# Kernel optimization log

Measured on AMD Instinct MI355X. Metric: run time of the kernel, lower is better.

## Reference

```python
import jax, jax.numpy as jnp
import numpy as np


def setup_inputs() -> dict:
    key = jax.random.key(0)
    k1, k2 = jax.random.split(key)
    B, H, W, C = 8, 192, 640, 64
    c1 = jax.random.normal(k1, (B, H, W, C), dtype=jnp.float32)
    warp = jax.random.normal(k2, (B, H, W, C), dtype=jnp.float32)
    return {"c1": c1, "warp": warp, "search_range": 2}


def reference(c1, warp, search_range):
    # c1, warp: [B, H, W, C]; pad warp along width by search_range on both sides
    padded = jnp.pad(warp, ((0, 0), (0, 0), (search_range, search_range), (0, 0)))
    width = c1.shape[2]
    max_offset = 2 * search_range + 1  # small fixed loop (5 offsets)
    cost_vol = [
        jnp.mean(c1 * padded[:, :, i:width + i, :], axis=3, keepdims=True)
        for i in range(max_offset)
    ]
    # cost_curve: [B, H, W, C + max_offset]
    return jnp.concatenate([c1] + cost_vol, axis=3)
```

## Files before the change

### kernel.cpp

```cpp
#include <hip/hip_runtime.h>


typedef float f32x4 __attribute__((ext_vector_type(4)));

#define WIDTH 640
#define CH 64
#define NOFF 5
#define OUTC 69
#define REC_F4 69
#define NPIX (8 * 192 * 640)
#define NPAIR (NPIX / 8)
#define NITER 8
#define BDIM 256
#define WPB (BDIM / 64)
#define NBLOCKS (NPAIR / (WPB * NITER))
#define PAIRS_PER_ROW (WIDTH / 8)

__device__ __forceinline__ float row_reduce_sum16_lane0(float v) {
    union { float f; int i; } a, b;
    a.f = v;
    b.i = __builtin_amdgcn_update_dpp(0, a.i, 0x101, 0xF, 0xF, true); a.f += b.f;
    b.i = __builtin_amdgcn_update_dpp(0, a.i, 0x102, 0xF, 0xF, true); a.f += b.f;
    b.i = __builtin_amdgcn_update_dpp(0, a.i, 0x104, 0xF, 0xF, true); a.f += b.f;
    b.i = __builtin_amdgcn_update_dpp(0, a.i, 0x108, 0xF, 0xF, true); a.f += b.f;
    return a.f;
}

struct Frag {
    f32x4 a0, a1;
    f32x4 b0[NOFF], b1[NOFF];
};

__global__ __launch_bounds__(BDIM) void StereoCostVolume_kernel(
    const float* __restrict__ c1,
    const float* __restrict__ warp,
    float* __restrict__ out)
{
    __shared__ f32x4 lds[WPB * 2 * REC_F4];

    const int t   = threadIdx.x;
    const int wid = t >> 6;
    const int l   = t & 63;
    const int px  = l >> 4;
    const int c4  = l & 15;

    const f32x4* c1f4   = (const f32x4*)c1;
    const f32x4* warpf4 = (const f32x4*)warp;
    f32x4*       outf4  = (f32x4*)out;

    const int wave  = blockIdx.x * WPB + wid;
    const int pbase = wave * NITER;
    const int rp0   = pbase % PAIRS_PER_ROW;
    const bool leftw  = (rp0 == 0);
    const bool rightw = (rp0 == PAIRS_PER_ROW - NITER);

    const int base0 = (pbase * 8 + px) * 16 + c4;

    float* rec0w = (float*)&lds[(wid * 2 + 0) * REC_F4];
    float* rec1w = (float*)&lds[(wid * 2 + 1) * REC_F4];
    const f32x4* rec0r = (const f32x4*)rec0w;
    const f32x4* rec1r = (const f32x4*)rec1w;

    auto LOAD = [&](int it, Frag& F) {
        const int base = base0 + it * 128;
        F.a0 = __builtin_nontemporal_load(&c1f4[base]);
        F.a1 = __builtin_nontemporal_load(&c1f4[base + 64]);
        const bool edge = (leftw && it == 0) || (rightw && it == NITER - 1);
        if (!edge) {
            #pragma unroll
            for (int d = 0; d < NOFF; ++d) {
                F.b0[d] = warpf4[base + (d - 2) * 16];
                F.b1[d] = warpf4[base + 64 + (d - 2) * 16];
            }
        } else {
            const int w0 = (rp0 + it) * 8 + px;
            #pragma unroll
            for (int d = 0; d < NOFF; ++d) {
                const int ww0 = w0 + d - 2;
                const int ww1 = ww0 + 4;
                F.b0[d] = (ww0 >= 0 && ww0 < WIDTH) ? warpf4[base + (d - 2) * 16]
                                                    : f32x4{0.f, 0.f, 0.f, 0.f};
                F.b1[d] = (ww1 >= 0 && ww1 < WIDTH) ? warpf4[base + 64 + (d - 2) * 16]
                                                    : f32x4{0.f, 0.f, 0.f, 0.f};
            }
        }
    };

    auto PROC = [&](int it, const Frag& F) {
        float s0[NOFF], s1[NOFF];
        #pragma unroll
        for (int d = 0; d < NOFF; ++d) {
            const float acc0 = F.a0.x * F.b0[d].x + F.a0.y * F.b0[d].y
                             + F.a0.z * F.b0[d].z + F.a0.w * F.b0[d].w;
            const float acc1 = F.a1.x * F.b1[d].x + F.a1.y * F.b1[d].y
                             + F.a1.z * F.b1[d].z + F.a1.w * F.b1[d].w;
            s0[d] = row_reduce_sum16_lane0(acc0);
            s1[d] = row_reduce_sum16_lane0(acc1);
        }
        const int fb = px * OUTC + c4 * 4;
        rec0w[fb + 0] = F.a0.x; rec0w[fb + 1] = F.a0.y;
        rec0w[fb + 2] = F.a0.z; rec0w[fb + 3] = F.a0.w;
        rec1w[fb + 0] = F.a1.x; rec1w[fb + 1] = F.a1.y;
        rec1w[fb + 2] = F.a1.z; rec1w[fb + 3] = F.a1.w;
        if (c4 == 0) {
            #pragma unroll
            for (int d = 0; d < NOFF; ++d) {
                rec0w[px * OUTC + CH + d] = s0[d] * 0.015625f;
                rec1w[px * OUTC + CH + d] = s1[d] * 0.015625f;
            }
        }
        __builtin_amdgcn_wave_barrier();

        const int ob = (pbase + it) * (2 * REC_F4);
        __builtin_nontemporal_store(rec0r[l], &outf4[ob + l]);
        __builtin_nontemporal_store(rec1r[l], &outf4[ob + REC_F4 + l]);
        if (l < REC_F4 - 64) {
            __builtin_nontemporal_store(rec0r[64 + l], &outf4[ob + 64 + l]);
            __builtin_nontemporal_store(rec1r[64 + l], &outf4[ob + REC_F4 + 64 + l]);
        }
        __builtin_amdgcn_wave_barrier();
    };

    Frag X, Y;
    LOAD(0, X);
    #pragma unroll
    for (int ii = 0; ii < NITER; ii += 2) {
        LOAD(ii + 1, Y);
        PROC(ii, X);
        if (ii + 2 < NITER) LOAD(ii + 2, X);
        PROC(ii + 1, Y);
    }
}

extern "C" void kernel_launch(void* const* d_in, const int* in_sizes, int n_in,
                              void* d_out, int out_size, void* d_ws, size_t ws_size,
                              hipStream_t stream) {
    const float* c1   = (const float*)d_in[0];
    const float* warp = (const float*)d_in[1];
    float* out = (float*)d_out;

    StereoCostVolume_kernel<<<NBLOCKS, BDIM, 0, stream>>>(c1, warp, out);
}
```

Baseline: 125.4 us.

## Issue loads via inline asm with manual vmcnt waits for explicit double-buffering

Replaces the compiler-generated global loads with inline-asm global_load_dwordx4 using immediate offsets. The per-iteration pipeline is now driven by explicit s_waitcnt vmcnt values and sched barriers, so the next fragment's loads stay in flight while the current one is processed. Edge loads are turned into clamped, always-valid addresses, and out-of-range fragments are zeroed after the load instead of being predicated. This gives up the nontemporal hint on c1 loads. The hand-counted vmcnt values must exactly match the number of outstanding loads and stores, so any miscount would corrupt data.

```diff
diff --git a/kernel.cpp b/kernel.cpp
--- a/kernel.cpp
+++ b/kernel.cpp
@@ -15,6 +15,11 @@
 #define WPB (BDIM / 64)
 #define NBLOCKS (NPAIR / (WPB * NITER))
 #define PAIRS_PER_ROW (WIDTH / 8)
+
+#define WAITV(N) do { \
+    asm volatile("s_waitcnt vmcnt(" #N ")" ::: "memory"); \
+    __builtin_amdgcn_sched_barrier(0); \
+} while (0)
 
 __device__ __forceinline__ float row_reduce_sum16_lane0(float v) {
     union { float f; int i; } a, b;
@@ -62,31 +67,50 @@
     const f32x4* rec1r = (const f32x4*)rec1w;
 
     auto LOAD = [&](int it, Frag& F) {
-        const int base = base0 + it * 128;
-        F.a0 = __builtin_nontemporal_load(&c1f4[base]);
-        F.a1 = __builtin_nontemporal_load(&c1f4[base + 64]);
+        const char* cb = (const char*)(c1f4 + base0 + it * 128);
+        const char* wb = (const char*)(warpf4 + base0 + it * 128);
+        asm volatile("global_load_dwordx4 %0, %1, off"             : "=v"(F.a0) : "v"(cb));
+        asm volatile("global_load_dwordx4 %0, %1, off offset:1024" : "=v"(F.a1) : "v"(cb));
         const bool edge = (leftw && it == 0) || (rightw && it == NITER - 1);
         if (!edge) {
-            #pragma unroll
-            for (int d = 0; d < NOFF; ++d) {
-                F.b0[d] = warpf4[base + (d - 2) * 16];
-                F.b1[d] = warpf4[base + 64 + (d - 2) * 16];
-            }
+            asm volatile("global_load_dwordx4 %0, %1, off offset:-512" : "=v"(F.b0[0]) : "v"(wb));
+            asm volatile("global_load_dwordx4 %0, %1, off offset:-256" : "=v"(F.b0[1]) : "v"(wb));
+            asm volatile("global_load_dwordx4 %0, %1, off"             : "=v"(F.b0[2]) : "v"(wb));
+            asm volatile("global_load_dwordx4 %0, %1, off offset:256"  : "=v"(F.b0[3]) : "v"(wb));
+            asm volatile("global_load_dwordx4 %0, %1, off offset:512"  : "=v"(F.b0[4]) : "v"(wb));
+            asm volatile("global_load_dwordx4 %0, %1, off offset:512"  : "=v"(F.b1[0]) : "v"(wb));
+            asm volatile("global_load_dwordx4 %0, %1, off offset:768"  : "=v"(F.b1[1]) : "v"(wb));
+            asm volatile("global_load_dwordx4 %0, %1, off offset:1024" : "=v"(F.b1[2]) : "v"(wb));
+            asm volatile("global_load_dwordx4 %0, %1, off offset:1280" : "=v"(F.b1[3]) : "v"(wb));
+            asm volatile("global_load_dwordx4 %0, %1, off offset:1536" : "=v"(F.b1[4]) : "v"(wb));
         } else {
             const int w0 = (rp0 + it) * 8 + px;
             #pragma unroll
             for (int d = 0; d < NOFF; ++d) {
                 const int ww0 = w0 + d - 2;
                 const int ww1 = ww0 + 4;
-                F.b0[d] = (ww0 >= 0 && ww0 < WIDTH) ? warpf4[base + (d - 2) * 16]
-                                                    : f32x4{0.f, 0.f, 0.f, 0.f};
-                F.b1[d] = (ww1 >= 0 && ww1 < WIDTH) ? warpf4[base + 64 + (d - 2) * 16]
-                                                    : f32x4{0.f, 0.f, 0.f, 0.f};
+                const int cl0 = ww0 < 0 ? 0 : (ww0 >= WIDTH ? WIDTH - 1 : ww0);
+                const int cl1 = ww1 < 0 ? 0 : (ww1 >= WIDTH ? WIDTH - 1 : ww1);
+                const f32x4* p0 = warpf4 + base0 + it * 128 + (cl0 - w0) * 16;
+                const f32x4* p1 = warpf4 + base0 + it * 128 + 64 + (cl1 - w0 - 4) * 16;
+                asm volatile("global_load_dwordx4 %0, %1, off" : "=v"(F.b0[d]) : "v"(p0));
+                asm volatile("global_load_dwordx4 %0, %1, off" : "=v"(F.b1[d]) : "v"(p1));
             }
         }
     };
 
-    auto PROC = [&](int it, const Frag& F) {
+    auto PROC = [&](int it, Frag& F) {
+        const bool edge = (leftw && it == 0) || (rightw && it == NITER - 1);
+        if (edge) {
+            const int w0 = (rp0 + it) * 8 + px;
+            #pragma unroll
+            for (int d = 0; d < NOFF; ++d) {
+                const int ww0 = w0 + d - 2;
+                const int ww1 = ww0 + 4;
+                if (ww0 < 0 || ww0 >= WIDTH) F.b0[d] = f32x4{0.f, 0.f, 0.f, 0.f};
+                if (ww1 < 0 || ww1 >= WIDTH) F.b1[d] = f32x4{0.f, 0.f, 0.f, 0.f};
+            }
+        }
         float s0[NOFF], s1[NOFF];
         #pragma unroll
         for (int d = 0; d < NOFF; ++d) {
@@ -123,13 +147,15 @@
 
     Frag X, Y;
     LOAD(0, X);
-    #pragma unroll
-    for (int ii = 0; ii < NITER; ii += 2) {
-        LOAD(ii + 1, Y);
-        PROC(ii, X);
-        if (ii + 2 < NITER) LOAD(ii + 2, X);
-        PROC(ii + 1, Y);
-    }
+    LOAD(1, Y);
+    WAITV(12); PROC(0, X);
+    LOAD(2, X); WAITV(16); PROC(1, Y);
+    LOAD(3, Y); WAITV(16); PROC(2, X);
+    LOAD(4, X); WAITV(16); PROC(3, Y);
+    LOAD(5, Y); WAITV(16); PROC(4, X);
+    LOAD(6, X); WAITV(16); PROC(5, Y);
+    LOAD(7, Y); WAITV(16); PROC(6, X);
+    WAITV(4);  PROC(7, Y);
 }
 
 extern "C" void kernel_launch(void* const* d_in, const int* in_sizes, int n_in,
```

Result: slower. 144.8 us (+15.4%).
